# Optimization experiments

Hardware: AMD Instinct MI355X
Metric: run time of the kernel (lower is better)

Reference implementation:

```python
import jax, jax.numpy as jnp
import numpy as np

N = 50000   # nodes
E = 200000  # edges per snapshot
T = 2       # temporal snapshots
IN = 64     # in_dim
H = 32      # h_dim
ED = 16     # edge_dim
Z = 32      # z_dim
S = 5       # neighbor samples


def setup_inputs() -> dict:
    key = jax.random.key(0)
    ks = jax.random.split(key, 20)
    g = lambda i, shape: jax.random.normal(ks[i], shape, jnp.float32) * 0.05
    return {
        "x": jax.random.normal(ks[0], (N, IN), jnp.float32),
        "ei0": jax.random.randint(ks[1], (2, E), 0, N, dtype=jnp.int32),
        "ea0": jax.random.normal(ks[2], (E, ED), jnp.float32),
        "ei1": jax.random.randint(ks[3], (2, E), 0, N, dtype=jnp.int32),
        "ea1": jax.random.normal(ks[4], (E, ED), jnp.float32),
        "idx": jnp.sort(jax.random.randint(ks[5], (N + 1,), 0, E, dtype=jnp.int32)),
        "ptr": jax.random.randint(ks[6], (E,), 0, N, dtype=jnp.int32),
        "W1": g(7, (IN, H)), "b1": jnp.zeros((H,), jnp.float32),
        "W2": g(8, (H, H)), "b2": jnp.zeros((H,), jnp.float32),
        "W3": g(9, (H, H)), "b3": jnp.zeros((H,), jnp.float32),
        "nnW1": g(10, (ED, 8)), "nnb1": jnp.zeros((8,), jnp.float32),
        "nnW2": g(11, (8, H * H)), "nnb2": jnp.zeros((H * H,), jnp.float32),
        "root": g(12, (H, H)), "cbias": jnp.zeros((H,), jnp.float32),
        "Wih": g(13, (3 * H, H)), "Whh": g(14, (3 * H, H)),
        "bih": jnp.zeros((3 * H,), jnp.float32), "bhh": jnp.zeros((3 * H,), jnp.float32),
        "Wlin": g(15, (H, Z)), "blin": jnp.zeros((Z,), jnp.float32),
        "Wdec": g(16, (Z, Z)), "bdec": jnp.zeros((Z,), jnp.float32),
    }


def _gcn(z, src, dst, W, b):
    # GCNConv with symmetric norm; self loops already in (src, dst)
    deg = jax.ops.segment_sum(jnp.ones_like(src, jnp.float32), dst, N)
    dinv = jnp.where(deg > 0, 1.0 / jnp.sqrt(jnp.maximum(deg, 1.0)), 0.0)
    h = z @ W
    msg = (dinv[src] * dinv[dst])[:, None] * h[src]
    return jax.ops.segment_sum(msg, dst, N) + b


def _nnconv(z, src, dst, ea, nnW1, nnb1, nnW2, nnb2, root, cbias):
    # edge MLP -> per-edge [H,H] weight, per-edge matvec, mean-scatter at dst
    We = (jax.nn.relu(ea @ nnW1 + nnb1) @ nnW2 + nnb2).reshape(-1, H, H)
    msg = jnp.einsum('eh,eho->eo', z[src], We)
    cnt = jax.ops.segment_sum(jnp.ones_like(src, jnp.float32), dst, N)
    agg = jax.ops.segment_sum(msg, dst, N) / jnp.maximum(cnt, 1.0)[:, None]
    return agg + z @ root + cbias


def _forward(x, ei0, ea0, ei1, ea1, idx, ptr,
             W1, b1, W2, b2, W3, b3, nnW1, nnb1, nnW2, nnb2, root, cbias,
             Wih, Whh, bih, bhh, Wlin, blin, Wdec, bdec):
    loops = jnp.arange(N, dtype=ei0.dtype)

    def snap(ei, ea):
        src, dst = ei[0], ei[1]
        ssl = jnp.concatenate([src, loops])
        dsl = jnp.concatenate([dst, loops])
        z = _gcn(x, ssl, dsl, W1, b1)                 # c1 (no act)
        z = jax.nn.relu(_gcn(z, ssl, dsl, W2, b2))    # c2 + relu (dropout=eval)
        z = jax.nn.relu(_gcn(z, ssl, dsl, W3, b3))    # c3 + relu
        return jnp.tanh(_nnconv(z, src, dst, ea, nnW1, nnb1, nnW2, nnb2, root, cbias))

    zs = jnp.stack([snap(ei0, ea0), snap(ei1, ea1)], axis=1)  # [N, T, H]

    # nn.GRU(batch_first=False) on [N, T, H]: scans over NODE axis, batch=T
    def step(h, xt):
        gi = xt @ Wih.T + bih
        gh = h @ Whh.T + bhh
        ir, iz, inn = jnp.split(gi, 3, axis=-1)
        hr, hz, hn = jnp.split(gh, 3, axis=-1)
        r = jax.nn.sigmoid(ir + hr)
        u = jax.nn.sigmoid(iz + hz)
        n = jnp.tanh(inn + r * hn)
        hnew = (1.0 - u) * n + u * h
        return hnew, hnew

    _, ys = jax.lax.scan(step, jnp.zeros((T, H), jnp.float32), zs)
    out = ys @ Wlin + blin  # [N, T, Z]

    # sample_z: uniform sample of S neighbors (with replacement) from CSR (idx, ptr)
    deg = (idx[1:] - idx[:-1]).astype(jnp.float32)  # [N]
    key = jax.random.key(42)
    res = []
    for t in range(T):
        u = jax.random.uniform(jax.random.fold_in(key, t), (N, S))
        j = jnp.floor(u * deg[:, None]).astype(idx.dtype)
        pos = jnp.clip(idx[:-1, None] + j, 0, E - 1)
        nb = ptr[pos]                               # [N, S] sampled neighbors
        zt = out[:, t, :]
        ag = (zt[nb].sum(axis=1) + zt) / (S + 1.0)
        ag = jnp.where((deg > 0)[:, None], ag, zt)  # no neighbors -> identity
        res.append(jax.nn.softmax(ag @ Wdec + bdec, axis=1))
    return jnp.stack(res)  # [T, N, Z]


def reference(x, ei0, ea0, ei1, ea1, idx, ptr,
              W1, b1, W2, b2, W3, b3, nnW1, nnb1, nnW2, nnb2, root, cbias,
              Wih, Whh, bih, bhh, Wlin, blin, Wdec, bdec):
    return _forward(x, ei0, ea0, ei1, ea1, idx, ptr,
                    W1, b1, W2, b2, W3, b3, nnW1, nnb1, nnW2, nnb2, root, cbias,
                    Wih, Whh, bih, bhh, Wlin, blin, Wdec, bdec)
```

## Files before the change

### kernel.cpp

```cpp
#include <hip/hip_runtime.h>
#include <stdint.h>

constexpr int NN = 50000;
constexpr int EE = 200000;
constexpr int N2 = 2*NN;
constexpr int E2 = 2*EE;
constexpr int GRU_WARM   = 24;
constexpr int GRU_CHUNKS = 2048;
constexpr int NB_SCAN = (N2 + 511) / 512;

#define DEVI __device__ __forceinline__

typedef float f32x2 __attribute__((ext_vector_type(2)));

DEVI uint32_t rotl32(uint32_t v, int d){ return (v<<d)|(v>>(32-d)); }

#define TFR(r) { x0 += x1; x1 = rotl32(x1, r); x1 ^= x0; }
DEVI void tf2x32(uint32_t k0, uint32_t k1, uint32_t x0, uint32_t x1,
                 uint32_t& o0, uint32_t& o1){
  uint32_t ks2 = k0 ^ k1 ^ 0x1BD11BDAu;
  x0 += k0; x1 += k1;
  TFR(13) TFR(15) TFR(26) TFR(6)
  x0 += k1;  x1 += ks2 + 1u;
  TFR(17) TFR(29) TFR(16) TFR(24)
  x0 += ks2; x1 += k0 + 2u;
  TFR(13) TFR(15) TFR(26) TFR(6)
  x0 += k0;  x1 += k1 + 3u;
  TFR(17) TFR(29) TFR(16) TFR(24)
  x0 += k1;  x1 += ks2 + 4u;
  TFR(13) TFR(15) TFR(26) TFR(6)
  x0 += ks2; x1 += k0 + 5u;
  o0 = x0; o1 = x1;
}

DEVI unsigned short bfr(float f){
  uint32_t u = __float_as_uint(f);
  return (unsigned short)((u + 0x7fffu + ((u >> 16) & 1u)) >> 16);
}
DEVI float bfi(unsigned short h){ return __uint_as_float(((uint32_t)h) << 16); }

DEVI uint32_t pk4f8(float a, float b, float c, float d){
  int r = 0;
  r = __builtin_amdgcn_cvt_pk_fp8_f32(a, b, r, false);
  r = __builtin_amdgcn_cvt_pk_fp8_f32(c, d, r, true);
  return (uint32_t)r;
}
DEVI float4 upk4f8(uint32_t u){
  f32x2 lo = __builtin_amdgcn_cvt_pk_f32_fp8((int)u, false);
  f32x2 hi = __builtin_amdgcn_cvt_pk_f32_fp8((int)u, true);
  return make_float4(lo.x, lo.y, hi.x, hi.y);
}
constexpr float P8SCALE = 64.0f;

template<int K, int ACTIN, int TRW, int EPI>
__global__ __launch_bounds__(256) void tgemm_k(
    const float* __restrict__ X, const float* __restrict__ Wg,
    const float* __restrict__ Bv, float* __restrict__ Y, float* __restrict__ Y2,
    const float* __restrict__ dinvB, const float* __restrict__ degB,
    const float* __restrict__ agg, unsigned short* __restrict__ Ybf,
    int rows, int Mt, int wld){
  __shared__ float xt[K*132];
  __shared__ float wl[K*32];
  const int gr = blockIdx.x, gy = blockIdx.y;
  #pragma unroll
  for (int p=0; p<K/8; p++){
    int flat = p*256 + threadIdx.x;
    int row  = flat / (K/4);
    int kq   = flat % (K/4);
    int grow = min(gr*128 + row, rows-1);
    float4 v = *(const float4*)(X + (size_t)grow*K + kq*4);
    if (ACTIN){ v.x=fmaxf(v.x,0.f); v.y=fmaxf(v.y,0.f); v.z=fmaxf(v.z,0.f); v.w=fmaxf(v.w,0.f); }
    xt[(kq*4+0)*132 + row] = v.x;
    xt[(kq*4+1)*132 + row] = v.y;
    xt[(kq*4+2)*132 + row] = v.z;
    xt[(kq*4+3)*132 + row] = v.w;
  }
  for (int i=threadIdx.x; i<K*32; i+=256){
    int k = i >> 5, c = i & 31;
    wl[i] = TRW ? Wg[(size_t)(gy*32+c)*wld + k] : Wg[(size_t)k*wld + gy*32 + c];
  }
  __syncthreads();
  const int tr4 = (threadIdx.x & 31) << 2;
  const int tc4 = (threadIdx.x >> 5) << 2;
  float acc[4][4] = {};
  #pragma unroll 8
  for (int k=0; k<K; k++){
    const float4 xv = *(const float4*)(xt + k*132 + tr4);
    const float4 wv = *(const float4*)(wl + (k<<5) + tc4);
    acc[0][0]=fmaf(xv.x,wv.x,acc[0][0]); acc[0][1]=fmaf(xv.x,wv.y,acc[0][1]);
    acc[0][2]=fmaf(xv.x,wv.z,acc[0][2]); acc[0][3]=fmaf(xv.x,wv.w,acc[0][3]);
    acc[1][0]=fmaf(xv.y,wv.x,acc[1][0]); acc[1][1]=fmaf(xv.y,wv.y,acc[1][1]);
    acc[1][2]=fmaf(xv.y,wv.z,acc[1][2]); acc[1][3]=fmaf(xv.y,wv.w,acc[1][3]);
    acc[2][0]=fmaf(xv.z,wv.x,acc[2][0]); acc[2][1]=fmaf(xv.z,wv.y,acc[2][1]);
    acc[2][2]=fmaf(xv.z,wv.z,acc[2][2]); acc[2][3]=fmaf(xv.z,wv.w,acc[2][3]);
    acc[3][0]=fmaf(xv.w,wv.x,acc[3][0]); acc[3][1]=fmaf(xv.w,wv.y,acc[3][1]);
    acc[3][2]=fmaf(xv.w,wv.z,acc[3][2]); acc[3][3]=fmaf(xv.w,wv.w,acc[3][3]);
  }
  const int cbase = gy*32 + tc4;
  float b4[4] = {0,0,0,0};
  if (Bv){ b4[0]=Bv[cbase]; b4[1]=Bv[cbase+1]; b4[2]=Bv[cbase+2]; b4[3]=Bv[cbase+3]; }
  #pragma unroll
  for (int i=0;i<4;i++){
    int r = gr*128 + tr4 + i;
    if (r >= rows) break;
    if (EPI == 0){
      float4 o = { acc[i][0]+b4[0], acc[i][1]+b4[1], acc[i][2]+b4[2], acc[i][3]+b4[3] };
      *(float4*)(Y + (size_t)r*Mt + cbase) = o;
    } else if (EPI == 1){
      float dv = dinvB[r];
      float4 hs = { dv*acc[i][0], dv*acc[i][1], dv*acc[i][2], dv*acc[i][3] };
      ushort4 u = { bfr(hs.x), bfr(hs.y), bfr(hs.z), bfr(hs.w) };
      *(ushort4*)(Ybf + ((size_t)r<<5) + tc4) = u;
      float4 o = { b4[0]+dv*hs.x, b4[1]+dv*hs.y, b4[2]+dv*hs.z, b4[3]+dv*hs.w };
      *(float4*)(Y2 + ((size_t)r<<5) + tc4) = o;
    } else if (EPI == 2){
      ushort4 u = { bfr(acc[i][0]), bfr(acc[i][1]), bfr(acc[i][2]), bfr(acc[i][3]) };
      *(ushort4*)(Ybf + (size_t)r*Mt + cbase) = u;
    } else if (EPI == 3){
      float inv = (1.0f/P8SCALE) / fmaxf(degB[r], 1.0f);
      const float4 ag = *(const float4*)(agg + ((size_t)r<<5) + tc4);
      float v0 = acc[i][0]+b4[0]+ag.x*inv;
      float v1 = acc[i][1]+b4[1]+ag.y*inv;
      float v2 = acc[i][2]+b4[2]+ag.z*inv;
      float v3 = acc[i][3]+b4[3]+ag.w*inv;
      float4 o;
      o.x = 1.0f - 2.0f/(__expf(2.0f*v0)+1.0f);
      o.y = 1.0f - 2.0f/(__expf(2.0f*v1)+1.0f);
      o.z = 1.0f - 2.0f/(__expf(2.0f*v2)+1.0f);
      o.w = 1.0f - 2.0f/(__expf(2.0f*v3)+1.0f);
      *(float4*)(Y + ((size_t)r<<5) + tc4) = o;
    } else if (EPI == 4){
      #pragma unroll
      for (int s=0;s<2;s++){
        int rr = r*2+s;
        float dv = dinvB[rr];
        float4 hs = { dv*acc[i][0], dv*acc[i][1], dv*acc[i][2], dv*acc[i][3] };
        ushort4 u = { bfr(hs.x), bfr(hs.y), bfr(hs.z), bfr(hs.w) };
        *(ushort4*)(Ybf + ((size_t)rr<<5) + tc4) = u;
        float4 o = { b4[0]+dv*hs.x, b4[1]+dv*hs.y, b4[2]+dv*hs.z, b4[3]+dv*hs.w };
        *(float4*)(Y2 + ((size_t)rr<<5) + tc4) = o;
      }
    } else {
      uint32_t u = pk4f8(acc[i][0]*P8SCALE, acc[i][1]*P8SCALE,
                         acc[i][2]*P8SCALE, acc[i][3]*P8SCALE);
      *(uint32_t*)((unsigned char*)Ybf + (size_t)r*Mt + cbase) = u;
    }
  }
}

__global__ void cnt_k(const int* __restrict__ ei0, const int* __restrict__ ei1,
                      int* __restrict__ cnt){
  int t = blockIdx.x*blockDim.x + threadIdx.x;
  if (t >= E2) return;
  int s = t >= EE;
  const int* ei = s ? ei1 : ei0;
  int e = t - s*EE;
  atomicAdd(cnt + ei[EE + e]*2 + s, 1);
}

__global__ __launch_bounds__(512) void scan1_k(const int* __restrict__ cnt,
                                               int* __restrict__ loc, int* __restrict__ bsum){
  int tid = threadIdx.x;
  int i = blockIdx.x*512 + tid;
  int v = (i < N2) ? cnt[i] : 0;
  int lane = tid & 63, w = tid >> 6;
  int s = v;
  #pragma unroll
  for (int d=1; d<64; d<<=1){ int o = __shfl_up(s, d); if (lane >= d) s += o; }
  __shared__ int wsum[8];
  if (lane == 63) wsum[w] = s;
  __syncthreads();
  int add = 0;
  #pragma unroll
  for (int k=0;k<8;k++) if (k < w) add += wsum[k];
  if (i < N2) loc[i] = add + s - v;
  if (tid == 511) bsum[blockIdx.x] = add + s;
}

__global__ __launch_bounds__(256) void scan2_k(int* __restrict__ bsum){
  int tid = threadIdx.x;
  int v = (tid < NB_SCAN) ? bsum[tid] : 0;
  int lane = tid & 63, w = tid >> 6;
  int s = v;
  #pragma unroll
  for (int d=1; d<64; d<<=1){ int o = __shfl_up(s, d); if (lane >= d) s += o; }
  __shared__ int wsum[4];
  if (lane == 63) wsum[w] = s;
  __syncthreads();
  int add = 0;
  #pragma unroll
  for (int k=0;k<4;k++) if (k < w) add += wsum[k];
  if (tid < NB_SCAN) bsum[tid] = add + s - v;
}

__global__ void scan3_k(const int* __restrict__ bsum, int* __restrict__ cursor,
                        int* __restrict__ rowptr, const int* __restrict__ cnt,
                        float* __restrict__ dinvB, float* __restrict__ degB){
  int i = blockIdx.x*blockDim.x + threadIdx.x;
  if (i < N2){
    int r = cursor[i] + bsum[i >> 9];
    rowptr[i] = r; cursor[i] = r;
    float c = (float)cnt[i];
    degB[i] = c; dinvB[i] = rsqrtf(c + 1.0f);
  }
  if (i == N2) rowptr[N2] = E2;
}

__global__ void fill_k(const int* __restrict__ ei0, const int* __restrict__ ei1,
                       int* __restrict__ cursor,
                       int* __restrict__ csr_src, int* __restrict__ csr_eid){
  int t = blockIdx.x*blockDim.x + threadIdx.x;
  if (t >= E2) return;
  int s = t >= EE;
  const int* ei = s ? ei1 : ei0;
  int e = t - s*EE;
  int d = ei[EE + e];
  int slot = atomicAdd(cursor + d*2 + s, 1);
  csr_src[slot] = ei[e]*2 + s;
  csr_eid[slot] = e;
}

__global__ __launch_bounds__(256) void temlp_k(const float* __restrict__ ea0,
    const float* __restrict__ ea1, const float* __restrict__ nnW1,
    const float* __restrict__ nnb1, unsigned short* __restrict__ tb){
  __shared__ float wt[136];
  for (int i=threadIdx.x; i<136; i+=256)
    wt[i] = (i < 128) ? nnW1[(i & 15)*8 + (i >> 4)] : nnb1[i - 128];
  __syncthreads();
  int t = blockIdx.x*256 + threadIdx.x;
  if (t >= E2) return;
  int s = t >= EE;
  const float* ea = s ? ea1 : ea0;
  int e = t - s*EE;
  const float4 a0 = *(const float4*)(ea + (size_t)e*16);
  const float4 a1 = *(const float4*)(ea + (size_t)e*16 + 4);
  const float4 a2 = *(const float4*)(ea + (size_t)e*16 + 8);
  const float4 a3 = *(const float4*)(ea + (size_t)e*16 + 12);
  unsigned short o8[8];
  #pragma unroll
  for (int m=0;m<8;m++){
    const float* wc = wt + m*16;
    float v = wt[128+m];
    v = fmaf(a0.x,wc[0], fmaf(a0.y,wc[1], fmaf(a0.z,wc[2], fmaf(a0.w,wc[3], v))));
    v = fmaf(a1.x,wc[4], fmaf(a1.y,wc[5], fmaf(a1.z,wc[6], fmaf(a1.w,wc[7], v))));
    v = fmaf(a2.x,wc[8], fmaf(a2.y,wc[9], fmaf(a2.z,wc[10],fmaf(a2.w,wc[11],v))));
    v = fmaf(a3.x,wc[12],fmaf(a3.y,wc[13],fmaf(a3.z,wc[14],fmaf(a3.w,wc[15],v))));
    o8[m] = bfr(fmaxf(v, 0.0f));
  }
  ushort4* tp = (ushort4*)(tb + (size_t)t*8);
  tp[0] = make_ushort4(o8[0],o8[1],o8[2],o8[3]);
  tp[1] = make_ushort4(o8[4],o8[5],o8[6],o8[7]);
}

__global__ __launch_bounds__(256) void gcngath_k(const unsigned short* __restrict__ hs,
    const float* __restrict__ dinvB, const int* __restrict__ rowptr,
    const int* __restrict__ csr_src, float* __restrict__ out){
  int t = blockIdx.x*256 + threadIdx.x;
  int n = t >> 3;
  if (n >= N2) return;
  int q = (t & 7) << 2;
  int b = rowptr[n], e = rowptr[n+1];
  float4 acc = {0,0,0,0};
  int p = b;
  for (; p + 2 <= e; p += 2){
    int s0 = csr_src[p], s1 = csr_src[p+1];
    ushort4 h0 = *(const ushort4*)(hs + ((size_t)s0<<5) + q);
    ushort4 h1 = *(const ushort4*)(hs + ((size_t)s1<<5) + q);
    acc.x += bfi(h0.x) + bfi(h1.x);
    acc.y += bfi(h0.y) + bfi(h1.y);
    acc.z += bfi(h0.z) + bfi(h1.z);
    acc.w += bfi(h0.w) + bfi(h1.w);
  }
  if (p < e){
    int s0 = csr_src[p];
    ushort4 h0 = *(const ushort4*)(hs + ((size_t)s0<<5) + q);
    acc.x += bfi(h0.x); acc.y += bfi(h0.y); acc.z += bfi(h0.z); acc.w += bfi(h0.w);
  }
  float dv = dinvB[n];
  float4 o = *(float4*)(out + ((size_t)n<<5) + q);
  o.x += dv*acc.x; o.y += dv*acc.y; o.z += dv*acc.z; o.w += dv*acc.w;
  *(float4*)(out + ((size_t)n<<5) + q) = o;
}

__global__ __launch_bounds__(256) void nngath_k(const unsigned char* __restrict__ P8,
    const unsigned short* __restrict__ tb,
    const int* __restrict__ rowptr, const int* __restrict__ csr_src,
    const int* __restrict__ csr_eid, float* __restrict__ agg){
  int t = blockIdx.x*256 + threadIdx.x;
  int n = t >> 3;
  if (n >= N2) return;
  int lane8 = threadIdx.x & 7;
  int ob = lane8 << 2;
  int sEE = (n & 1) ? EE : 0;
  int b = rowptr[n], e = rowptr[n+1];
  float4 acc = {0,0,0,0};
  int p = b;
  for (; p + 2 <= e; p += 2){
    int v0 = csr_src[p],   e0 = csr_eid[p];
    int v1 = csr_src[p+1], e1 = csr_eid[p+1];
    const unsigned char* pr0 = P8 + (size_t)v0*288 + ob;
    const unsigned char* pr1 = P8 + (size_t)v1*288 + ob;
    uint32_t u0[9], u1[9];
    #pragma unroll
    for (int k=0;k<9;k++) u0[k] = *(const uint32_t*)(pr0 + k*32);
    #pragma unroll
    for (int k=0;k<9;k++) u1[k] = *(const uint32_t*)(pr1 + k*32);
    ushort4 ta0 = *(const ushort4*)(tb + (size_t)(sEE + e0)*8);
    ushort4 tb0 = *(const ushort4*)(tb + (size_t)(sEE + e0)*8 + 4);
    ushort4 ta1 = *(const ushort4*)(tb + (size_t)(sEE + e1)*8);
    ushort4 tb1 = *(const ushort4*)(tb + (size_t)(sEE + e1)*8 + 4);
    float tc0[8] = { bfi(ta0.x),bfi(ta0.y),bfi(ta0.z),bfi(ta0.w),
                     bfi(tb0.x),bfi(tb0.y),bfi(tb0.z),bfi(tb0.w) };
    float tc1[8] = { bfi(ta1.x),bfi(ta1.y),bfi(ta1.z),bfi(ta1.w),
                     bfi(tb1.x),bfi(tb1.y),bfi(tb1.z),bfi(tb1.w) };
    float4 m0 = upk4f8(u0[0]);
    float4 m1 = upk4f8(u1[0]);
    #pragma unroll
    for (int k=0;k<8;k++){
      float4 q0 = upk4f8(u0[k+1]);
      m0.x = fmaf(tc0[k], q0.x, m0.x);
      m0.y = fmaf(tc0[k], q0.y, m0.y);
      m0.z = fmaf(tc0[k], q0.z, m0.z);
      m0.w = fmaf(tc0[k], q0.w, m0.w);
      float4 q1 = upk4f8(u1[k+1]);
      m1.x = fmaf(tc1[k], q1.x, m1.x);
      m1.y = fmaf(tc1[k], q1.y, m1.y);
      m1.z = fmaf(tc1[k], q1.z, m1.z);
      m1.w = fmaf(tc1[k], q1.w, m1.w);
    }
    acc.x += m0.x + m1.x; acc.y += m0.y + m1.y;
    acc.z += m0.z + m1.z; acc.w += m0.w + m1.w;
  }
  if (p < e){
    int v0 = csr_src[p], e0 = csr_eid[p];
    const unsigned char* pr0 = P8 + (size_t)v0*288 + ob;
    uint32_t u0[9];
    #pragma unroll
    for (int k=0;k<9;k++) u0[k] = *(const uint32_t*)(pr0 + k*32);
    ushort4 ta0 = *(const ushort4*)(tb + (size_t)(sEE + e0)*8);
    ushort4 tb0 = *(const ushort4*)(tb + (size_t)(sEE + e0)*8 + 4);
    float tc0[8] = { bfi(ta0.x),bfi(ta0.y),bfi(ta0.z),bfi(ta0.w),
                     bfi(tb0.x),bfi(tb0.y),bfi(tb0.z),bfi(tb0.w) };
    float4 m0 = upk4f8(u0[0]);
    #pragma unroll
    for (int k=0;k<8;k++){
      float4 q0 = upk4f8(u0[k+1]);
      m0.x = fmaf(tc0[k], q0.x, m0.x);
      m0.y = fmaf(tc0[k], q0.y, m0.y);
      m0.z = fmaf(tc0[k], q0.z, m0.z);
      m0.w = fmaf(tc0[k], q0.w, m0.w);
    }
    acc.x += m0.x; acc.y += m0.y; acc.z += m0.z; acc.w += m0.w;
  }
  *(float4*)(agg + ((size_t)n<<5) + ob) = acc;
}

__global__ void wprep_k(const float* __restrict__ nnW2, const float* __restrict__ nnb2,
                        const float* __restrict__ Wlin, const float* __restrict__ blin,
                        const float* __restrict__ Wdec, const float* __restrict__ bdec,
                        float* __restrict__ Wbig, float* __restrict__ Wp,
                        float* __restrict__ bp){
  int i = blockIdx.x*blockDim.x + threadIdx.x;
  if (i < 32*288){
    int j = i / 288, m = i - j*288, k = m >> 5, o = m & 31;
    Wbig[i] = (k == 0) ? nnb2[j*32 + o] : nnW2[(size_t)(k-1)*1024 + j*32 + o];
  } else if (i < 32*288 + 1024){
    int ii = i - 32*288;
    int k = ii >> 5, m = ii & 31;
    float s = 0.0f;
    #pragma unroll 8
    for (int j=0;j<32;j++) s = fmaf(Wlin[k*32+j], Wdec[j*32+m], s);
    Wp[ii] = s;
  } else if (i < 32*288 + 1056){
    int m = i - 32*288 - 1024;
    float s = bdec[m];
    #pragma unroll 8
    for (int j=0;j<32;j++) s = fmaf(blin[j], Wdec[j*32+m], s);
    bp[m] = s;
  }
}

__global__ __launch_bounds__(64) __attribute__((amdgpu_waves_per_eu(1, 2)))
void gru_k(const float* __restrict__ gi,
    const float* __restrict__ Whh, const float* __restrict__ bhh,
    float* __restrict__ ys, int L){
  __shared__ float hl[64];
  int lane = threadIdx.x;
  int j = lane & 31, t = lane >> 5;
  int start = blockIdx.x * L;
  if (start >= NN) return;
  int end = min(start + L, NN);
  int n0 = max(0, start - GRU_WARM);
  float wr[32], wz[32], wn[32];
  #pragma unroll
  for (int k=0;k<32;k++) wr[k] = Whh[j*32 + k];
  #pragma unroll
  for (int k=0;k<32;k++) wz[k] = Whh[(32+j)*32 + k];
  #pragma unroll
  for (int k=0;k<32;k++) wn[k] = Whh[(64+j)*32 + k];
  #pragma unroll
  for (int k=0;k<32;k++)
    asm volatile("" : "+v"(wr[k]), "+v"(wz[k]), "+v"(wn[k]));
  float br = bhh[j], bz = bhh[32+j], bn = bhh[64+j];
  float h = 0.0f;
  hl[lane] = 0.0f;
  const float* g0 = gi + ((size_t)n0*2 + t)*96;
  float c0 = g0[j], c1 = g0[32+j], c2 = g0[64+j];
  const float* hb = hl + (t << 5);
  for (int n = n0; n < end; n++){
    int np = (n+1 < end) ? n+1 : n;
    const float* gp = gi + ((size_t)np*2 + t)*96;
    float p0 = gp[j], p1 = gp[32+j], p2 = gp[64+j];
    float ar = br, az = bz, an = bn;
    #pragma unroll
    for (int kk=0; kk<8; kk++){
      const float4 h4 = *(const float4*)(hb + (kk<<2));
      ar = fmaf(h4.x, wr[kk*4+0], ar); az = fmaf(h4.x, wz[kk*4+0], az); an = fmaf(h4.x, wn[kk*4+0], an);
      ar = fmaf(h4.y, wr[kk*4+1], ar); az = fmaf(h4.y, wz[kk*4+1], az); an = fmaf(h4.y, wn[kk*4+1], an);
      ar = fmaf(h4.z, wr[kk*4+2], ar); az = fmaf(h4.z, wz[kk*4+2], az); an = fmaf(h4.z, wn[kk*4+2], an);
      ar = fmaf(h4.w, wr[kk*4+3], ar); az = fmaf(h4.w, wz[kk*4+3], az); an = fmaf(h4.w, wn[kk*4+3], an);
    }
    float r = 1.0f/(1.0f + __expf(-(c0+ar)));
    float u = 1.0f/(1.0f + __expf(-(c1+az)));
    float pre = c2 + r*an;
    float e2 = __expf(2.0f*pre);
    float nn2 = 1.0f - 2.0f/(e2 + 1.0f);
    h = (1.0f-u)*nn2 + u*h;
    hl[lane] = h;
    if (n >= start) ys[((size_t)n << 6) + lane] = h;
    c0 = p0; c1 = p1; c2 = p2;
  }
}

__global__ __launch_bounds__(256) void final_k(const unsigned short* __restrict__ Lp,
    const int* __restrict__ idx, const int* __restrict__ ptr,
    float* __restrict__ dout){
  int grp = blockIdx.x*8 + (threadIdx.x >> 5);
  if (grp >= N2) return;
  int o = threadIdx.x & 31;
  int lane = threadIdx.x & 63;
  int t = (grp >= NN) ? 1 : 0;
  int n = grp - (t ? NN : 0);
  int i0 = idx[n], i1 = idx[n+1];
  float degf = (float)(i1 - i0);
  int nb = 0;
  {
    uint32_t fk0, fk1;
    tf2x32(0u, 42u, 0u, (uint32_t)t, fk0, fk1);
    int sidx = (o < 5) ? o : 4;
    uint32_t b = (uint32_t)(n*5 + sidx);
    bool hi = (b >= 125000u);
    uint32_t pair = hi ? (b - 125000u) : b;
    uint32_t r0, r1;
    tf2x32(fk0, fk1, pair, pair + 125000u, r0, r1);
    uint32_t bits = hi ? r1 : r0;
    float u = __uint_as_float((bits >> 9) | 0x3f800000u) - 1.0f;
    int jj = (int)floorf(u * degf);
    int pos = i0 + jj;
    pos = min(max(pos, 0), EE - 1);
    nb = ptr[pos];
  }
  float lo = bfi(Lp[((size_t)(n*2 + t) << 5) + o]);
  if (degf > 0.0f){
    float ssum = lo;
    #pragma unroll
    for (int s5=0;s5<5;s5++){
      int ns = __shfl(nb, (lane & 32) | s5);
      ssum += bfi(Lp[((size_t)(ns*2 + t) << 5) + o]);
    }
    lo = ssum * (1.0f/6.0f);
  }
  float m = lo;
  #pragma unroll
  for (int d5=16; d5>0; d5>>=1) m = fmaxf(m, __shfl_xor(m, d5));
  float ex = __expf(lo - m);
  float sum = ex;
  #pragma unroll
  for (int d5=16; d5>0; d5>>=1) sum += __shfl_xor(sum, d5);
  dout[((size_t)t*NN + n)*32 + o] = ex / sum;
}

static inline int g256(int n){ return (n + 255) / 256; }

extern "C" void kernel_launch(void* const* d_in, const int* in_sizes, int n_in,
                              void* d_out, int out_size, void* d_ws, size_t ws_size,
                              hipStream_t stream){
  const float* x    = (const float*)d_in[0];
  const int*   ei0  = (const int*)  d_in[1];
  const float* ea0  = (const float*)d_in[2];
  const int*   ei1  = (const int*)  d_in[3];
  const float* ea1  = (const float*)d_in[4];
  const int*   idx  = (const int*)  d_in[5];
  const int*   ptr  = (const int*)  d_in[6];
  const float* W1   = (const float*)d_in[7];
  const float* b1   = (const float*)d_in[8];
  const float* W2   = (const float*)d_in[9];
  const float* b2   = (const float*)d_in[10];
  const float* W3   = (const float*)d_in[11];
  const float* b3   = (const float*)d_in[12];
  const float* nnW1 = (const float*)d_in[13];
  const float* nnb1 = (const float*)d_in[14];
  const float* nnW2 = (const float*)d_in[15];
  const float* nnb2 = (const float*)d_in[16];
  const float* root = (const float*)d_in[17];
  const float* cbias= (const float*)d_in[18];
  const float* Wih  = (const float*)d_in[19];
  const float* Whh  = (const float*)d_in[20];
  const float* bih  = (const float*)d_in[21];
  const float* bhh  = (const float*)d_in[22];
  const float* Wlin = (const float*)d_in[23];
  const float* blin = (const float*)d_in[24];
  const float* Wdec = (const float*)d_in[25];
  const float* bdec = (const float*)d_in[26];

  float* ws = (float*)d_ws;
  size_t off = 0;
  float* degB = ws + off; off += N2;
  float* dinvB= ws + off; off += N2;
  float* Wbig = ws + off; off += 32*288;
  float* Wp   = ws + off; off += 1024;
  float* bp   = ws + off; off += 32;
  int*   ib   = (int*)(ws + off); off += 1200000;
  unsigned short* tbuf = (unsigned short*)(ws + off); off += 1600000;
  float* A    = ws + off; off += (size_t)N2*32;
  float* B    = ws + off; off += (size_t)N2*32;
  float* C    = ws + off; off += (size_t)N2*32;
  float* D    = ws + off; off += (size_t)N2*80;
  unsigned short* hbf = (unsigned short*)D;
  unsigned char*  P8  = (unsigned char*)D;
  float* gib  = B;
  float* ys   = D + (size_t)N2*32;
  unsigned short* Lp = (unsigned short*)A;

  int* cnt     = ib;
  int* rowptr  = ib + N2;
  int* cursor  = ib + 2*N2 + 1;
  int* bsum    = ib + 3*N2 + 1;
  int* csr_src = ib + 3*N2 + 1 + 256;
  int* csr_eid = csr_src + E2;

  const dim3 gN1(( NN + 127)/128, 1);
  const dim3 gB1((N2 + 127)/128, 1), gB3((N2 + 127)/128, 3);
  const dim3 gP9((N2 + 127)/128, 9);

  wprep_k<<<g256(32*288 + 1056), 256, 0, stream>>>(nnW2, nnb2, Wlin, blin, Wdec, bdec,
                                                   Wbig, Wp, bp);
  temlp_k<<<g256(E2), 256, 0, stream>>>(ea0, ea1, nnW1, nnb1, tbuf);

  hipMemsetAsync(cnt, 0, N2*sizeof(int), stream);
  cnt_k <<<g256(E2), 256, 0, stream>>>(ei0, ei1, cnt);
  scan1_k<<<NB_SCAN, 512, 0, stream>>>(cnt, cursor, bsum);
  scan2_k<<<1, 256, 0, stream>>>(bsum);
  scan3_k<<<g256(N2+1), 256, 0, stream>>>(bsum, cursor, rowptr, cnt, dinvB, degB);
  fill_k<<<g256(E2), 256, 0, stream>>>(ei0, ei1, cursor, csr_src, csr_eid);

  tgemm_k<64,0,0,4><<<gN1, 256, 0, stream>>>(x, W1, b1, nullptr, B, dinvB, nullptr, nullptr, hbf, NN, 32, 32);
  gcngath_k<<<g256(N2*8), 256, 0, stream>>>(hbf, dinvB, rowptr, csr_src, B);
  tgemm_k<32,0,0,1><<<gB1, 256, 0, stream>>>(B, W2, b2, nullptr, C, dinvB, nullptr, nullptr, hbf, N2, 32, 32);
  gcngath_k<<<g256(N2*8), 256, 0, stream>>>(hbf, dinvB, rowptr, csr_src, C);
  tgemm_k<32,1,0,1><<<gB1, 256, 0, stream>>>(C, W3, b3, nullptr, B, dinvB, nullptr, nullptr, hbf, N2, 32, 32);
  gcngath_k<<<g256(N2*8), 256, 0, stream>>>(hbf, dinvB, rowptr, csr_src, B);
  tgemm_k<32,1,0,5><<<gP9, 256, 0, stream>>>(B, Wbig, nullptr, nullptr, nullptr, nullptr, nullptr, nullptr, (unsigned short*)P8, N2, 288, 288);
  nngath_k<<<g256(N2*8), 256, 0, stream>>>(P8, tbuf, rowptr, csr_src, csr_eid, C);
  tgemm_k<32,1,0,3><<<gB1, 256, 0, stream>>>(B, root, cbias, A, nullptr, nullptr, degB, C, nullptr, N2, 32, 32);
  tgemm_k<32,0,1,0><<<gB3, 256, 0, stream>>>(A, Wih, bih, gib, nullptr, nullptr, nullptr, nullptr, nullptr, N2, 96, 32);
  int L = (NN + GRU_CHUNKS - 1) / GRU_CHUNKS;
  gru_k<<<GRU_CHUNKS, 64, 0, stream>>>(gib, Whh, bhh, ys, L);
  tgemm_k<32,0,0,2><<<gB1, 256, 0, stream>>>(ys, Wp, bp, nullptr, nullptr, nullptr, nullptr, nullptr, Lp, N2, 32, 32);
  final_k<<<(N2 + 7)/8, 256, 0, stream>>>(Lp, idx, ptr, (float*)d_out);
}
```

Baseline: 312.5 us.

## Fuse root GEMM into edge-weight GEMM and store GRU input gates in bf16

Appends the NNConv root weight as a tenth column block of the per-node weight-projection matrix. A new pgemm kernel loads each X tile once and produces both the fp8 per-edge weight projections and the root term, replacing the 9-block tgemm launch and the separate root GEMM. A small elementwise kernel then applies bias, mean aggregation and tanh. The GRU input-gate projections are now written and read as bf16 instead of fp32, which roughly halves that traffic but lowers precision and moves bias addition into the EPI 2 epilogue.

Measured after the change: 313.7 us. Within noise of the previous version (+0.4%).

```diff
diff --git a/kernel.cpp b/kernel.cpp
--- a/kernel.cpp
+++ b/kernel.cpp
@@ -56,8 +56,7 @@
 __global__ __launch_bounds__(256) void tgemm_k(
     const float* __restrict__ X, const float* __restrict__ Wg,
     const float* __restrict__ Bv, float* __restrict__ Y, float* __restrict__ Y2,
-    const float* __restrict__ dinvB, const float* __restrict__ degB,
-    const float* __restrict__ agg, unsigned short* __restrict__ Ybf,
+    const float* __restrict__ dinvB, unsigned short* __restrict__ Ybf,
     int rows, int Mt, int wld){
   __shared__ float xt[K*132];
   __shared__ float wl[K*32];
@@ -114,22 +113,10 @@
       float4 o = { b4[0]+dv*hs.x, b4[1]+dv*hs.y, b4[2]+dv*hs.z, b4[3]+dv*hs.w };
       *(float4*)(Y2 + ((size_t)r<<5) + tc4) = o;
     } else if (EPI == 2){
-      ushort4 u = { bfr(acc[i][0]), bfr(acc[i][1]), bfr(acc[i][2]), bfr(acc[i][3]) };
+      ushort4 u = { bfr(acc[i][0]+b4[0]), bfr(acc[i][1]+b4[1]),
+                    bfr(acc[i][2]+b4[2]), bfr(acc[i][3]+b4[3]) };
       *(ushort4*)(Ybf + (size_t)r*Mt + cbase) = u;
-    } else if (EPI == 3){
-      float inv = (1.0f/P8SCALE) / fmaxf(degB[r], 1.0f);
-      const float4 ag = *(const float4*)(agg + ((size_t)r<<5) + tc4);
-      float v0 = acc[i][0]+b4[0]+ag.x*inv;
-      float v1 = acc[i][1]+b4[1]+ag.y*inv;
-      float v2 = acc[i][2]+b4[2]+ag.z*inv;
-      float v3 = acc[i][3]+b4[3]+ag.w*inv;
-      float4 o;
-      o.x = 1.0f - 2.0f/(__expf(2.0f*v0)+1.0f);
-      o.y = 1.0f - 2.0f/(__expf(2.0f*v1)+1.0f);
-      o.z = 1.0f - 2.0f/(__expf(2.0f*v2)+1.0f);
-      o.w = 1.0f - 2.0f/(__expf(2.0f*v3)+1.0f);
-      *(float4*)(Y + ((size_t)r<<5) + tc4) = o;
-    } else if (EPI == 4){
+    } else {
       #pragma unroll
       for (int s=0;s<2;s++){
         int rr = r*2+s;
@@ -140,12 +127,83 @@
         float4 o = { b4[0]+dv*hs.x, b4[1]+dv*hs.y, b4[2]+dv*hs.z, b4[3]+dv*hs.w };
         *(float4*)(Y2 + ((size_t)rr<<5) + tc4) = o;
       }
-    } else {
-      uint32_t u = pk4f8(acc[i][0]*P8SCALE, acc[i][1]*P8SCALE,
-                         acc[i][2]*P8SCALE, acc[i][3]*P8SCALE);
-      *(uint32_t*)((unsigned char*)Ybf + (size_t)r*Mt + cbase) = u;
     }
   }
+}
+
+__global__ __launch_bounds__(256) void pgemm_k(const float* __restrict__ X,
+    const float* __restrict__ Wbig2, unsigned char* __restrict__ P8,
+    float* __restrict__ R, int rows){
+  __shared__ float xt[32*132];
+  __shared__ float wl[32*320];
+  const int gr = blockIdx.x;
+  #pragma unroll
+  for (int p=0; p<4; p++){
+    int flat = p*256 + threadIdx.x;
+    int row = flat >> 3, kq = flat & 7;
+    int grow = min(gr*128 + row, rows-1);
+    float4 v = *(const float4*)(X + (size_t)grow*32 + kq*4);
+    v.x=fmaxf(v.x,0.f); v.y=fmaxf(v.y,0.f); v.z=fmaxf(v.z,0.f); v.w=fmaxf(v.w,0.f);
+    xt[(kq*4+0)*132 + row] = v.x;
+    xt[(kq*4+1)*132 + row] = v.y;
+    xt[(kq*4+2)*132 + row] = v.z;
+    xt[(kq*4+3)*132 + row] = v.w;
+  }
+  for (int i=threadIdx.x; i<(32*320/4); i+=256)
+    ((float4*)wl)[i] = ((const float4*)Wbig2)[i];
+  __syncthreads();
+  const int tr4 = (threadIdx.x & 31) << 2;
+  const int tc4 = (threadIdx.x >> 5) << 2;
+  for (int gy=0; gy<10; gy++){
+    float acc[4][4] = {};
+    #pragma unroll 8
+    for (int k=0; k<32; k++){
+      const float4 xv = *(const float4*)(xt + k*132 + tr4);
+      const float4 wv = *(const float4*)(wl + k*320 + gy*32 + tc4);
+      acc[0][0]=fmaf(xv.x,wv.x,acc[0][0]); acc[0][1]=fmaf(xv.x,wv.y,acc[0][1]);
+      acc[0][2]=fmaf(xv.x,wv.z,acc[0][2]); acc[0][3]=fmaf(xv.x,wv.w,acc[0][3]);
+      acc[1][0]=fmaf(xv.y,wv.x,acc[1][0]); acc[1][1]=fmaf(xv.y,wv.y,acc[1][1]);
+      acc[1][2]=fmaf(xv.y,wv.z,acc[1][2]); acc[1][3]=fmaf(xv.y,wv.w,acc[1][3]);
+      acc[2][0]=fmaf(xv.z,wv.x,acc[2][0]); acc[2][1]=fmaf(xv.z,wv.y,acc[2][1]);
+      acc[2][2]=fmaf(xv.z,wv.z,acc[2][2]); acc[2][3]=fmaf(xv.z,wv.w,acc[2][3]);
+      acc[3][0]=fmaf(xv.w,wv.x,acc[3][0]); acc[3][1]=fmaf(xv.w,wv.y,acc[3][1]);
+      acc[3][2]=fmaf(xv.w,wv.z,acc[3][2]); acc[3][3]=fmaf(xv.w,wv.w,acc[3][3]);
+    }
+    #pragma unroll
+    for (int i=0;i<4;i++){
+      int r = gr*128 + tr4 + i;
+      if (r >= rows) break;
+      if (gy < 9){
+        uint32_t u = pk4f8(acc[i][0]*P8SCALE, acc[i][1]*P8SCALE,
+                           acc[i][2]*P8SCALE, acc[i][3]*P8SCALE);
+        *(uint32_t*)(P8 + (size_t)r*288 + gy*32 + tc4) = u;
+      } else {
+        float4 o = { acc[i][0], acc[i][1], acc[i][2], acc[i][3] };
+        *(float4*)(R + ((size_t)r<<5) + tc4) = o;
+      }
+    }
+  }
+}
+
+__global__ void zsfin_k(float* __restrict__ R, const float* __restrict__ agg,
+                        const float* __restrict__ degB, const float* __restrict__ cbias){
+  int t = blockIdx.x*blockDim.x + threadIdx.x;
+  if (t >= N2*8) return;
+  int n = t >> 3, q = (t & 7) << 2;
+  float inv = (1.0f/P8SCALE) / fmaxf(degB[n], 1.0f);
+  const float4 ag = *(const float4*)(agg + ((size_t)n<<5) + q);
+  float4 v = *(const float4*)(R + ((size_t)n<<5) + q);
+  const float* cb = cbias + q;
+  v.x = v.x + cb[0] + ag.x*inv;
+  v.y = v.y + cb[1] + ag.y*inv;
+  v.z = v.z + cb[2] + ag.z*inv;
+  v.w = v.w + cb[3] + ag.w*inv;
+  float4 o;
+  o.x = 1.0f - 2.0f/(__expf(2.0f*v.x)+1.0f);
+  o.y = 1.0f - 2.0f/(__expf(2.0f*v.y)+1.0f);
+  o.z = 1.0f - 2.0f/(__expf(2.0f*v.z)+1.0f);
+  o.w = 1.0f - 2.0f/(__expf(2.0f*v.w)+1.0f);
+  *(float4*)(R + ((size_t)n<<5) + q) = o;
 }
 
 __global__ void cnt_k(const int* __restrict__ ei0, const int* __restrict__ ei1,
@@ -356,23 +414,28 @@
 }
 
 __global__ void wprep_k(const float* __restrict__ nnW2, const float* __restrict__ nnb2,
+                        const float* __restrict__ root,
                         const float* __restrict__ Wlin, const float* __restrict__ blin,
                         const float* __restrict__ Wdec, const float* __restrict__ bdec,
-                        float* __restrict__ Wbig, float* __restrict__ Wp,
+                        float* __restrict__ Wbig2, float* __restrict__ Wp,
                         float* __restrict__ bp){
   int i = blockIdx.x*blockDim.x + threadIdx.x;
-  if (i < 32*288){
-    int j = i / 288, m = i - j*288, k = m >> 5, o = m & 31;
-    Wbig[i] = (k == 0) ? nnb2[j*32 + o] : nnW2[(size_t)(k-1)*1024 + j*32 + o];
-  } else if (i < 32*288 + 1024){
-    int ii = i - 32*288;
+  if (i < 32*320){
+    int j = i / 320, m = i - j*320;
+    float v;
+    if (m >= 288)      v = root[j*32 + (m - 288)];
+    else { int k = m >> 5, o = m & 31;
+           v = (k == 0) ? nnb2[j*32 + o] : nnW2[(size_t)(k-1)*1024 + j*32 + o]; }
+    Wbig2[i] = v;
+  } else if (i < 32*320 + 1024){
+    int ii = i - 32*320;
     int k = ii >> 5, m = ii & 31;
     float s = 0.0f;
     #pragma unroll 8
     for (int j=0;j<32;j++) s = fmaf(Wlin[k*32+j], Wdec[j*32+m], s);
     Wp[ii] = s;
-  } else if (i < 32*288 + 1056){
-    int m = i - 32*288 - 1024;
+  } else if (i < 32*320 + 1056){
+    int m = i - 32*320 - 1024;
     float s = bdec[m];
     #pragma unroll 8
     for (int j=0;j<32;j++) s = fmaf(blin[j], Wdec[j*32+m], s);
@@ -381,7 +444,7 @@
 }
 
 __global__ __launch_bounds__(64) __attribute__((amdgpu_waves_per_eu(1, 2)))
-void gru_k(const float* __restrict__ gi,
+void gru_k(const unsigned short* __restrict__ gi16,
     const float* __restrict__ Whh, const float* __restrict__ bhh,
     float* __restrict__ ys, int L){
   __shared__ float hl[64];
@@ -404,13 +467,13 @@
   float br = bhh[j], bz = bhh[32+j], bn = bhh[64+j];
   float h = 0.0f;
   hl[lane] = 0.0f;
-  const float* g0 = gi + ((size_t)n0*2 + t)*96;
-  float c0 = g0[j], c1 = g0[32+j], c2 = g0[64+j];
+  const unsigned short* g0 = gi16 + ((size_t)n0*2 + t)*96;
+  float c0 = bfi(g0[j]), c1 = bfi(g0[32+j]), c2 = bfi(g0[64+j]);
   const float* hb = hl + (t << 5);
   for (int n = n0; n < end; n++){
     int np = (n+1 < end) ? n+1 : n;
-    const float* gp = gi + ((size_t)np*2 + t)*96;
-    float p0 = gp[j], p1 = gp[32+j], p2 = gp[64+j];
+    const unsigned short* gp = gi16 + ((size_t)np*2 + t)*96;
+    float p0 = bfi(gp[j]), p1 = bfi(gp[32+j]), p2 = bfi(gp[64+j]);
     float ar = br, az = bz, an = bn;
     #pragma unroll
     for (int kk=0; kk<8; kk++){
@@ -517,7 +580,7 @@
   size_t off = 0;
   float* degB = ws + off; off += N2;
   float* dinvB= ws + off; off += N2;
-  float* Wbig = ws + off; off += 32*288;
+  float* Wbig2= ws + off; off += 32*320;
   float* Wp   = ws + off; off += 1024;
   float* bp   = ws + off; off += 32;
   int*   ib   = (int*)(ws + off); off += 1200000;
@@ -528,8 +591,8 @@
   float* D    = ws + off; off += (size_t)N2*80;
   unsigned short* hbf = (unsigned short*)D;
   unsigned char*  P8  = (unsigned char*)D;
-  float* gib  = B;
-  float* ys   = D + (size_t)N2*32;
+  unsigned short* gi16 = (unsigned short*)B;
+  float* ys   = D;
   unsigned short* Lp = (unsigned short*)A;
 
   int* cnt     = ib;
@@ -541,10 +604,9 @@
 
   const dim3 gN1(( NN + 127)/128, 1);
   const dim3 gB1((N2 + 127)/128, 1), gB3((N2 + 127)/128, 3);
-  const dim3 gP9((N2 + 127)/128, 9);
-
-  wprep_k<<<g256(32*288 + 1056), 256, 0, stream>>>(nnW2, nnb2, Wlin, blin, Wdec, bdec,
-                                                   Wbig, Wp, bp);
+
+  wprep_k<<<g256(32*320 + 1056), 256, 0, stream>>>(nnW2, nnb2, root, Wlin, blin,
+                                                   Wdec, bdec, Wbig2, Wp, bp);
   temlp_k<<<g256(E2), 256, 0, stream>>>(ea0, ea1, nnW1, nnb1, tbuf);
 
   hipMemsetAsync(cnt, 0, N2*sizeof(int), stream);
@@ -554,18 +616,18 @@
   scan3_k<<<g256(N2+1), 256, 0, stream>>>(bsum, cursor, rowptr, cnt, dinvB, degB);
   fill_k<<<g256(E2), 256, 0, stream>>>(ei0, ei1, cursor, csr_src, csr_eid);
 
-  tgemm_k<64,0,0,4><<<gN1, 256, 0, stream>>>(x, W1, b1, nullptr, B, dinvB, nullptr, nullptr, hbf, NN, 32, 32);
+  tgemm_k<64,0,0,4><<<gN1, 256, 0, stream>>>(x, W1, b1, nullptr, B, dinvB, hbf, NN, 32, 32);
   gcngath_k<<<g256(N2*8), 256, 0, stream>>>(hbf, dinvB, rowptr, csr_src, B);
-  tgemm_k<32,0,0,1><<<gB1, 256, 0, stream>>>(B, W2, b2, nullptr, C, dinvB, nullptr, nullptr, hbf, N2, 32, 32);
+  tgemm_k<32,0,0,1><<<gB1, 256, 0, stream>>>(B, W2, b2, nullptr, C, dinvB, hbf, N2, 32, 32);
   gcngath_k<<<g256(N2*8), 256, 0, stream>>>(hbf, dinvB, rowptr, csr_src, C);
-  tgemm_k<32,1,0,1><<<gB1, 256, 0, stream>>>(C, W3, b3, nullptr, B, dinvB, nullptr, nullptr, hbf, N2, 32, 32);
+  tgemm_k<32,1,0,1><<<gB1, 256, 0, stream>>>(C, W3, b3, nullptr, B, dinvB, hbf, N2, 32, 32);
   gcngath_k<<<g256(N2*8), 256, 0, stream>>>(hbf, dinvB, rowptr, csr_src, B);
-  tgemm_k<32,1,0,5><<<gP9, 256, 0, stream>>>(B, Wbig, nullptr, nullptr, nullptr, nullptr, nullptr, nullptr, (unsigned short*)P8, N2, 288, 288);
+  pgemm_k<<<gB1, 256, 0, stream>>>(B, Wbig2, P8, A, N2);
   nngath_k<<<g256(N2*8), 256, 0, stream>>>(P8, tbuf, rowptr, csr_src, csr_eid, C);
-  tgemm_k<32,1,0,3><<<gB1, 256, 0, stream>>>(B, root, cbias, A, nullptr, nullptr, degB, C, nullptr, N2, 32, 32);
-  tgemm_k<32,0,1,0><<<gB3, 256, 0, stream>>>(A, Wih, bih, gib, nullptr, nullptr, nullptr, nullptr, nullptr, N2, 96, 32);
+  zsfin_k<<<g256(N2*8), 256, 0, stream>>>(A, C, degB, cbias);
+  tgemm_k<32,0,1,2><<<gB3, 256, 0, stream>>>(A, Wih, bih, nullptr, nullptr, nullptr, gi16, N2, 96, 32);
   int L = (NN + GRU_CHUNKS - 1) / GRU_CHUNKS;
-  gru_k<<<GRU_CHUNKS, 64, 0, stream>>>(gib, Whh, bhh, ys, L);
-  tgemm_k<32,0,0,2><<<gB1, 256, 0, stream>>>(ys, Wp, bp, nullptr, nullptr, nullptr, nullptr, nullptr, Lp, N2, 32, 32);
+  gru_k<<<GRU_CHUNKS, 64, 0, stream>>>(gi16, Whh, bhh, ys, L);
+  tgemm_k<32,0,0,2><<<gB1, 256, 0, stream>>>(ys, Wp, bp, nullptr, nullptr, nullptr, Lp, N2, 32, 32);
   final_k<<<(N2 + 7)/8, 256, 0, stream>>>(Lp, idx, ptr, (float*)d_out);
 }
```
